# Performance work log

Measured on AMD Instinct MI355X. Metric: run time of the kernel, lower is better.

The kernel has to match this reference:

```python
import jax, jax.numpy as jnp
import numpy as np

IN_CH, OUT_CH = 384, 512


def setup_inputs() -> dict:
    key = jax.random.key(0)
    ks = jax.random.split(key, 9)
    B, C, H, W = 8, IN_CH, 48, 48
    s_in = 1.0 / np.sqrt(IN_CH)
    s_out = 1.0 / np.sqrt(OUT_CH)
    return {
        "x": jax.random.normal(ks[0], (B, C, H, W), dtype=jnp.float32),
        "Wq": jax.random.uniform(ks[1], (OUT_CH, IN_CH), jnp.float32, -s_in, s_in),
        "bq": jax.random.uniform(ks[2], (OUT_CH,), jnp.float32, -s_in, s_in),
        "Wk": jax.random.uniform(ks[3], (OUT_CH, IN_CH), jnp.float32, -s_in, s_in),
        "bk": jax.random.uniform(ks[4], (OUT_CH,), jnp.float32, -s_in, s_in),
        "Wv": jax.random.uniform(ks[5], (OUT_CH, IN_CH), jnp.float32, -s_in, s_in),
        "bv": jax.random.uniform(ks[6], (OUT_CH,), jnp.float32, -s_in, s_in),
        "Wo": jax.random.uniform(ks[7], (OUT_CH, OUT_CH), jnp.float32, -s_out, s_out),
        "bo": jax.random.uniform(ks[8], (OUT_CH,), jnp.float32, -s_out, s_out),
    }


def reference(x, Wq, bq, Wk, bk, Wv, bv, Wo, bo):
    B, C, H, W = x.shape
    N = H * W  # number of spatial tokens
    xf = x.reshape(B, C, N)  # [B, C, N]
    # 1x1 convs == per-pixel linear projections
    q = jnp.einsum('oc,bcn->bno', Wq, xf) + bq  # [B, N, O]
    k = jnp.einsum('oc,bcn->bon', Wk, xf) + bk[None, :, None]  # [B, O, N]
    v = jnp.einsum('oc,bcn->bon', Wv, xf) + bv[None, :, None]  # [B, O, N]
    scale = 1.0 / jnp.sqrt(jnp.asarray(Wq.shape[0], x.dtype))
    attn = jax.nn.softmax(jnp.einsum('bno,bom->bnm', q, k) * scale, axis=-1)  # [B, N, N]
    out = jnp.einsum('bom,bnm->bon', v, attn)  # [B, O, N]
    out = jnp.einsum('po,bon->bpn', Wo, out) + bo[None, :, None]
    return out.reshape(B, Wo.shape[0], H, W)
```

## Files before the change

kernel.cpp:

```cpp
#include <hip/hip_runtime.h>
#include <stdint.h>

#define B_    8
#define CIN   384
#define OCH   512
#define NTOK  2304
#define SCALE 0.044194173824159216f

typedef unsigned short u16;
typedef u16   u16x8 __attribute__((ext_vector_type(8)));
typedef short s16x8 __attribute__((ext_vector_type(8)));
typedef float f32x4 __attribute__((ext_vector_type(4)));

__device__ __forceinline__ u16 f2bf(float f) {
    union { uint32_t i; float f; } v; v.f = f;
    uint32_t r = v.i + 0x7fffu + ((v.i >> 16) & 1u);
    return (u16)(r >> 16);
}

typedef __attribute__((address_space(1))) const uint32_t glb_u32;
typedef __attribute__((address_space(3))) uint32_t lds_u32;

__device__ __forceinline__ void gld16(const u16* g, u16* l) {
    __builtin_amdgcn_global_load_lds((glb_u32*)g, (lds_u32*)l, 16, 0, 0);
}

__device__ __forceinline__ size_t baddr(int row, int col, int Kc) {
    return ((size_t)(row >> 4) * (Kc >> 5) + (col >> 5)) * 512
         + (size_t)(((col >> 3) & 3) * 128 + (row & 15) * 8 + (col & 7));
}

__device__ __forceinline__ void stage_blocked(const u16* __restrict__ base,
                                              int row0, int k0, int Kc,
                                              u16* __restrict__ dst, int t)
{
    const int lane = t & 63;
    const int w = t >> 6;
    const int bpr = Kc >> 5;
#pragma unroll
    for (int it = 0; it < 2; ++it) {
        const int ck = w * 2 + it;
        const u16* gp = base + ((size_t)((row0 >> 4) + ck) * bpr + (k0 >> 5)) * 512
                      + (size_t)lane * 8;
        u16* lp = dst + ck * 512;
        __builtin_amdgcn_global_load_lds((glb_u32*)gp, (lds_u32*)lp, 16, 0, 0);
    }
}

__device__ __forceinline__ void mfma_core(const u16* __restrict__ As,
                                          const u16* __restrict__ Bs,
                                          int wm16, int wn16, int lrow, int kq,
                                          f32x4 acc[4][4])
{
    s16x8 a[4], b[4];
#pragma unroll
    for (int i = 0; i < 4; ++i)
        a[i] = *(const s16x8*)(As + (((wm16 + i) * 64) + kq * 16 + lrow) * 8);
#pragma unroll
    for (int j = 0; j < 4; ++j)
        b[j] = *(const s16x8*)(Bs + (((wn16 + j) * 64) + kq * 16 + lrow) * 8);
#pragma unroll
    for (int i = 0; i < 4; ++i)
#pragma unroll
        for (int j = 0; j < 4; ++j)
            acc[i][j] = __builtin_amdgcn_mfma_f32_16x16x32_bf16(a[i], b[j], acc[i][j], 0, 0, 0);
}

template <int MODE, int K>
__device__ __forceinline__ void gemm64_core(
    u16* __restrict__ sm,
    const u16* __restrict__ A, const u16* __restrict__ Bp,
    const float* __restrict__ aux, void* __restrict__ Cout,
    int N, int m0, int n0)
{
    constexpr int NT = K / 32;
    u16* As0 = sm;
    u16* Bs0 = sm + 2048;
    u16* As1 = sm + 4096;
    u16* Bs1 = sm + 6144;

    const int ln = threadIdx.x & 63;
    const int lrow = ln & 15, kq = ln >> 4;

    const int bpr = K >> 5;
    const size_t rstep = (size_t)bpr << 9;
    const u16* pA = A  + (((size_t)(m0 >> 4) * bpr) << 9) + (size_t)(ln << 3);
    const u16* pB = Bp + (((size_t)(n0 >> 4) * bpr) << 9) + (size_t)(ln << 3);

    f32x4 acc[4][4] = {};

#define STAGE8(ga, gb, Ad, Bd)                                             \
    gld16((ga),             (Ad));        gld16((ga) + rstep,     (Ad) + 512);  \
    gld16((ga) + 2 * rstep, (Ad) + 1024); gld16((ga) + 3 * rstep, (Ad) + 1536); \
    gld16((gb),             (Bd));        gld16((gb) + rstep,     (Bd) + 512);  \
    gld16((gb) + 2 * rstep, (Bd) + 1024); gld16((gb) + 3 * rstep, (Bd) + 1536);

    STAGE8(pA, pB, As0, Bs0)

#pragma unroll 1
    for (int kt = 0; kt < NT; kt += 2) {
        STAGE8(pA + 512, pB + 512, As1, Bs1)
        asm volatile("s_waitcnt vmcnt(8)" ::: "memory");
        mfma_core(As0, Bs0, 0, 0, lrow, kq, acc);
        asm volatile("" ::: "memory");
        if (kt + 2 < NT) {
            STAGE8(pA + 1024, pB + 1024, As0, Bs0)
            asm volatile("s_waitcnt vmcnt(8)" ::: "memory");
        } else {
            asm volatile("s_waitcnt vmcnt(0)" ::: "memory");
        }
        mfma_core(As1, Bs1, 0, 0, lrow, kq, acc);
        asm volatile("" ::: "memory");
        pA += 1024; pB += 1024;
    }
#undef STAGE8

    const int offl = ((lrow >> 3) << 7) + (lrow & 7) + (kq << 5);

    if constexpr (MODE == 1) {
        u16* C = (u16*)Cout;
        float bcol[4];
#pragma unroll
        for (int j = 0; j < 4; ++j) bcol[j] = aux[n0 + j * 16 + lrow];
#pragma unroll
        for (int i = 0; i < 4; ++i) {
            u16* Crow = C + ((size_t)((m0 >> 4) + i) * (N >> 5) + (n0 >> 5)) * 512 + offl;
#pragma unroll
            for (int j = 0; j < 4; ++j) {
                u16* Cj = Crow + (j >> 1) * 512 + ((j & 1) << 8);
#pragma unroll
                for (int r = 0; r < 4; ++r)
                    Cj[r * 8] = f2bf(acc[i][j][r] + bcol[j]);
            }
        }
    } else if constexpr (MODE == 2) {
        u16* C = (u16*)Cout;
#pragma unroll
        for (int i = 0; i < 4; ++i) {
            const float4 b4 = *(const float4*)(aux + m0 + i * 16 + kq * 4);
            u16* Crow = C + ((size_t)((m0 >> 4) + i) * (N >> 5) + (n0 >> 5)) * 512 + offl;
#pragma unroll
            for (int j = 0; j < 4; ++j) {
                u16* Cj = Crow + (j >> 1) * 512 + ((j & 1) << 8);
                Cj[0]  = f2bf(acc[i][j][0] + b4.x);
                Cj[8]  = f2bf(acc[i][j][1] + b4.y);
                Cj[16] = f2bf(acc[i][j][2] + b4.z);
                Cj[24] = f2bf(acc[i][j][3] + b4.w);
            }
        }
    } else {
        float* C = (float*)Cout;
#pragma unroll
        for (int i = 0; i < 4; ++i) {
            const int row = m0 + i * 16 + kq * 4;
            const float4 b4 = *(const float4*)(aux + row);
            const float bv4[4] = {b4.x, b4.y, b4.z, b4.w};
#pragma unroll
            for (int r = 0; r < 4; ++r)
#pragma unroll
                for (int j = 0; j < 4; ++j)
                    C[(size_t)(row + r) * N + n0 + j * 16 + lrow] = acc[i][j][r] + bv4[r];
        }
    }
}

#define WQKV_SZ (OCH * CIN)
#define WO_SZ   (OCH * OCH)
#define CH_QKV  (WQKV_SZ / 8)
#define CH_WO   (WO_SZ / 8)
#define CH_TOT  (3 * CH_QKV + CH_WO)
#define PREP_BLK (CH_TOT / 256)
#define TRX_BLK  ((NTOK / 64) * (CIN / 64) * B_)

__global__ __launch_bounds__(256) void prep_kernel(
    const float* __restrict__ Wq, const float* __restrict__ Wk,
    const float* __restrict__ Wv, const float* __restrict__ Wo,
    u16* __restrict__ Wqb, u16* __restrict__ Wkb,
    u16* __restrict__ Wvb, u16* __restrict__ Wob,
    const float* __restrict__ x, u16* __restrict__ xT)
{
    __shared__ float Ts[64][66];
    const int t = threadIdx.x;

    if (blockIdx.x < PREP_BLK) {
        int lc = blockIdx.x * 256 + t;
        const float* src; u16* dst; int Kc;
        if      (lc < CH_QKV)     { src = Wq; dst = Wqb; Kc = CIN; }
        else if (lc < 2 * CH_QKV) { src = Wk; dst = Wkb; Kc = CIN; lc -= CH_QKV; }
        else if (lc < 3 * CH_QKV) { src = Wv; dst = Wvb; Kc = CIN; lc -= 2 * CH_QKV; }
        else                      { src = Wo; dst = Wob; Kc = OCH; lc -= 3 * CH_QKV; }
        const int brick = lc >> 6, l = lc & 63;
        const int bpr = Kc >> 5;
        const int g = brick / bpr, c = brick % bpr;
        const int row = g * 16 + (l & 15);
        const int col = c * 32 + (l >> 4) * 8;
        const float* s = src + (size_t)row * Kc + col;
        float4 v0 = *(const float4*)s;
        float4 v1 = *(const float4*)(s + 4);
        u16x8 o;
        o[0] = f2bf(v0.x); o[1] = f2bf(v0.y); o[2] = f2bf(v0.z); o[3] = f2bf(v0.w);
        o[4] = f2bf(v1.x); o[5] = f2bf(v1.y); o[6] = f2bf(v1.z); o[7] = f2bf(v1.w);
        *(u16x8*)(dst + (size_t)lc * 8) = o;
        return;
    }

    const int tb = blockIdx.x - PREP_BLK;
    const int n0 = (tb % 36) * 64;
    const int c0 = ((tb / 36) % 6) * 64;
    const int b  = tb / 216;
    const float* X = x + (size_t)b * CIN * NTOK;

#pragma unroll
    for (int rep = 0; rep < 4; ++rep) {
        const int cr = (t >> 4) + rep * 16;
        const int n4 = (t & 15) * 4;
        float4 v = *(const float4*)(X + (size_t)(c0 + cr) * NTOK + n0 + n4);
        *(float2*)&Ts[cr][n4]     = make_float2(v.x, v.y);
        *(float2*)&Ts[cr][n4 + 2] = make_float2(v.z, v.w);
    }
    __syncthreads();

    u16* O = xT + (size_t)b * NTOK * CIN;
#pragma unroll
    for (int rep = 0; rep < 2; ++rep) {
        const int nr = (t >> 3) + rep * 32;
        const int c8 = (t & 7) * 8;
        u16 tmp[8];
#pragma unroll
        for (int j = 0; j < 8; ++j) tmp[j] = f2bf(Ts[c8 + j][nr]);
        *(u16x8*)(O + baddr(n0 + nr, c0 + c8, CIN)) = *(const u16x8*)tmp;
    }
}

__global__ __launch_bounds__(64) void qkv64_kernel(
    const u16* __restrict__ xT,
    const u16* __restrict__ Wqb, const float* __restrict__ bq,
    const u16* __restrict__ Wkb, const float* __restrict__ bk,
    const u16* __restrict__ Wvb, const float* __restrict__ bv,
    u16* __restrict__ Qt, u16* __restrict__ Kt, u16* __restrict__ Vw)
{
    __shared__ __align__(16) u16 sm[8192];
    const int sel = blockIdx.x % 24;
    const int b = sel & 7, which = sel >> 3;
    const int rem = blockIdx.x / 24;
    const u16* xTb = xT + (size_t)b * NTOK * CIN;
    if (which < 2) {
        const int n0 = (rem & 7) * 64, m0 = (rem >> 3) * 64;
        gemm64_core<1, CIN>(sm, xTb, which ? Wkb : Wqb, which ? bk : bq,
            (which ? Kt : Qt) + (size_t)b * NTOK * OCH, OCH, m0, n0);
    } else {
        const int n0 = (rem % 36) * 64, m0 = (rem / 36) * 64;
        gemm64_core<2, CIN>(sm, Wvb, xTb, bv,
            Vw + (size_t)b * OCH * NTOK, NTOK, m0, n0);
    }
}

__global__ __launch_bounds__(256) void logits_exp_kernel(
    const u16* __restrict__ Qt, const u16* __restrict__ Kt,
    u16* __restrict__ Ew, float* __restrict__ rowsumG)
{
    const int z   = blockIdx.x % B_;
    const int rem = blockIdx.x / B_;
    const int n0 = (rem % (NTOK / 128)) * 128;
    const int m0 = (rem / (NTOK / 128)) * 128;
    const u16* A  = Qt + (size_t)z * NTOK * OCH;
    const u16* Bp = Kt + (size_t)z * NTOK * OCH;

    __shared__ u16 As[128 * 32];
    __shared__ u16 Bs[128 * 32];
    __shared__ float rowsumL[128];

    const int t = threadIdx.x;
    const int w = t >> 6, ln = t & 63;
    const int wm16 = (w & 1) * 4, wn16 = (w >> 1) * 4;
    const int lrow = ln & 15, kq = ln >> 4;

    if (t < 128) rowsumL[t] = 0.f;

    f32x4 acc[4][4] = {};

    for (int k0 = 0; k0 < OCH; k0 += 32) {
        stage_blocked(A, m0, k0, OCH, As, t);
        stage_blocked(Bp, n0, k0, OCH, Bs, t);
        __syncthreads();
        mfma_core(As, Bs, wm16, wn16, lrow, kq, acc);
        __syncthreads();
    }

    u16* E = Ew + (size_t)z * NTOK * NTOK;
    const int offl = ((lrow >> 3) << 7) + (lrow & 7) + (kq << 5);
#pragma unroll
    for (int i = 0; i < 4; ++i) {
        u16* Erow = E + ((size_t)((m0 >> 4) + wm16 + i) * (NTOK >> 5) + (n0 >> 5)) * 512 + offl;
#pragma unroll
        for (int r = 0; r < 4; ++r) {
            float part = 0.f;
#pragma unroll
            for (int j = 0; j < 4; ++j) {
                float e = __expf(acc[i][j][r] * SCALE);
                part += e;
                Erow[((wn16 + j) >> 1) * 512 + ((j & 1) << 8) + r * 8] = f2bf(e);
            }
            part += __shfl_xor(part, 1);
            part += __shfl_xor(part, 2);
            part += __shfl_xor(part, 4);
            part += __shfl_xor(part, 8);
            if (lrow == 0) atomicAdd(&rowsumL[(wm16 + i) * 16 + kq * 4 + r], part);
        }
    }
    __syncthreads();
    if (t < 128) atomicAdd(&rowsumG[(size_t)z * NTOK + m0 + t], rowsumL[t]);
}

__global__ __launch_bounds__(256) void pv_div_kernel(
    const u16* __restrict__ Ew, const u16* __restrict__ Vw,
    const float* __restrict__ rowsumG, u16* __restrict__ AOt)
{
    const int z   = blockIdx.x % B_;
    const int rem = blockIdx.x / B_;
    const int n0 = (rem % 4) * 128;
    const int m0 = (rem / 4) * 128;
    const u16* A  = Ew + (size_t)z * NTOK * NTOK;
    const u16* Bp = Vw + (size_t)z * OCH * NTOK;

    __shared__ u16 As[128 * 32];
    __shared__ u16 Bs[128 * 32];

    const int t = threadIdx.x;
    const int w = t >> 6, ln = t & 63;
    const int wm16 = (w & 1) * 4, wn16 = (w >> 1) * 4;
    const int lrow = ln & 15, kq = ln >> 4;

    f32x4 acc[4][4] = {};

    for (int k0 = 0; k0 < NTOK; k0 += 32) {
        stage_blocked(A, m0, k0, NTOK, As, t);
        stage_blocked(Bp, n0, k0, NTOK, Bs, t);
        __syncthreads();
        mfma_core(As, Bs, wm16, wn16, lrow, kq, acc);
        __syncthreads();
    }

    u16* AO = AOt + (size_t)z * NTOK * OCH;
    const int offl = ((lrow >> 3) << 7) + (lrow & 7) + (kq << 5);
#pragma unroll
    for (int i = 0; i < 4; ++i) {
        const float4 rs4 = *(const float4*)(rowsumG + (size_t)z * NTOK + m0 + (wm16 + i) * 16 + kq * 4);
        const float inv0 = 1.0f / rs4.x, inv1 = 1.0f / rs4.y;
        const float inv2 = 1.0f / rs4.z, inv3 = 1.0f / rs4.w;
        u16* Crow = AO + ((size_t)((m0 >> 4) + wm16 + i) * (OCH >> 5) + (n0 >> 5)) * 512 + offl;
#pragma unroll
        for (int j = 0; j < 4; ++j) {
            u16* Cj = Crow + ((wn16 + j) >> 1) * 512 + ((j & 1) << 8);
            Cj[0]  = f2bf(acc[i][j][0] * inv0);
            Cj[8]  = f2bf(acc[i][j][1] * inv1);
            Cj[16] = f2bf(acc[i][j][2] * inv2);
            Cj[24] = f2bf(acc[i][j][3] * inv3);
        }
    }
}

__global__ __launch_bounds__(64) void out64_kernel(
    const u16* __restrict__ Wob, const u16* __restrict__ AOt,
    const float* __restrict__ bo, float* __restrict__ out)
{
    __shared__ __align__(16) u16 sm[8192];
    const int z = blockIdx.x & 7;
    const int rem = blockIdx.x >> 3;
    const int n0 = (rem % 36) * 64, m0 = (rem / 36) * 64;
    gemm64_core<4, OCH>(sm, Wob, AOt + (size_t)z * NTOK * OCH, bo,
        out + (size_t)z * OCH * NTOK, NTOK, m0, n0);
}

extern "C" void kernel_launch(void* const* d_in, const int* in_sizes, int n_in,
                              void* d_out, int out_size, void* d_ws, size_t ws_size,
                              hipStream_t stream)
{
    const float* x  = (const float*)d_in[0];
    const float* Wq = (const float*)d_in[1];
    const float* bq = (const float*)d_in[2];
    const float* Wk = (const float*)d_in[3];
    const float* bk = (const float*)d_in[4];
    const float* Wv = (const float*)d_in[5];
    const float* bv = (const float*)d_in[6];
    const float* Wo = (const float*)d_in[7];
    const float* bo = (const float*)d_in[8];
    float* out = (float*)d_out;

    u16* ws = (u16*)d_ws;
    u16* Wqb = ws;
    u16* Wkb = Wqb + WQKV_SZ;
    u16* Wvb = Wkb + WQKV_SZ;
    u16* Wob = Wvb + WQKV_SZ;
    u16* xT  = Wob + WO_SZ;
    const size_t xtsz  = (size_t)B_ * NTOK * CIN;
    const size_t qkvsz = (size_t)B_ * NTOK * OCH;
    u16* Qt  = xT + xtsz;
    u16* Kt  = Qt + qkvsz;
    u16* Vw  = Kt + qkvsz;
    u16* Ew  = Vw + qkvsz;
    float* rowsumG = (float*)(Ew + (size_t)B_ * NTOK * NTOK);
    u16* AOt = Qt;

    dim3 blk(256), blk64(64);

    hipMemsetAsync(rowsumG, 0, (size_t)B_ * NTOK * sizeof(float), stream);

    prep_kernel<<<dim3(PREP_BLK + TRX_BLK), blk, 0, stream>>>(
        Wq, Wk, Wv, Wo, Wqb, Wkb, Wvb, Wob, x, xT);

    qkv64_kernel<<<dim3(288 * 24), blk64, 0, stream>>>(
        xT, Wqb, bq, Wkb, bk, Wvb, bv, Qt, Kt, Vw);

    logits_exp_kernel<<<dim3(18 * 18 * B_), blk, 0, stream>>>(Qt, Kt, Ew, rowsumG);

    pv_div_kernel<<<dim3(4 * 18 * B_), blk, 0, stream>>>(Ew, Vw, rowsumG, AOt);

    out64_kernel<<<dim3(288 * 8), blk64, 0, stream>>>(Wob, AOt, bo, out);
}
```

Measured before the change: 270.2 us.

## Rewrite logits kernel with 256x128 tiles, triple-buffered async LDS loads

Replaces the 128x128 logits/exp kernel with a 512-thread, 256x128-tile version. Global loads go directly to LDS through global_load_lds into three rotating buffers, prefetching two K-steps ahead and interleaving the loads with the MFMA phases under explicit waitcnt and barriers. It also raises wave priority around the MFMA bursts. The aim is to hide load latency and cut the per-step sync overhead of the old load-sync-compute loop, at the cost of about 144KB of LDS and more barriers.

```diff
diff --git a/kernel.cpp b/kernel.cpp
--- a/kernel.cpp
+++ b/kernel.cpp
@@ -255,61 +255,139 @@
     }
 }
 
-__global__ __launch_bounds__(256) void logits_exp_kernel(
+__global__ __launch_bounds__(512) void logits8p_kernel(
     const u16* __restrict__ Qt, const u16* __restrict__ Kt,
     u16* __restrict__ Ew, float* __restrict__ rowsumG)
 {
-    const int z   = blockIdx.x % B_;
-    const int rem = blockIdx.x / B_;
-    const int n0 = (rem % (NTOK / 128)) * 128;
-    const int m0 = (rem / (NTOK / 128)) * 128;
-    const u16* A  = Qt + (size_t)z * NTOK * OCH;
-    const u16* Bp = Kt + (size_t)z * NTOK * OCH;
-
-    __shared__ u16 As[128 * 32];
-    __shared__ u16 Bs[128 * 32];
-    __shared__ float rowsumL[128];
+    __shared__ __align__(16) u16 lds[3 * 24576];
+    __shared__ float rowsumL[256];
+
+    const int z = blockIdx.x & 7;
+    const int rem = blockIdx.x >> 3;
+    const int n0 = (rem % 18) * 128;
+    const int m0 = (rem / 18) * 256;
+    const u16* A = Qt + (size_t)z * NTOK * OCH;
+    const u16* B = Kt + (size_t)z * NTOK * OCH;
 
     const int t = threadIdx.x;
     const int w = t >> 6, ln = t & 63;
-    const int wm16 = (w & 1) * 4, wn16 = (w >> 1) * 4;
+    const int wr = w >> 2, wc = w & 3;
     const int lrow = ln & 15, kq = ln >> 4;
-
-    if (t < 128) rowsumL[t] = 0.f;
-
-    f32x4 acc[4][4] = {};
-
-    for (int k0 = 0; k0 < OCH; k0 += 32) {
-        stage_blocked(A, m0, k0, OCH, As, t);
-        stage_blocked(Bp, n0, k0, OCH, Bs, t);
-        __syncthreads();
-        mfma_core(As, Bs, wm16, wn16, lrow, kq, acc);
-        __syncthreads();
-    }
+    const int fo = (kq * 16 + lrow) * 8;
+
+    if (t < 256) rowsumL[t] = 0.f;
+
+    constexpr int NT = OCH / 64;
+    constexpr int bpr = OCH >> 5;
+    const int g0 = t >> 7;
+    const int cc = (t >> 6) & 1;
+    const int ll = t & 63;
+    const u16* gA = A + (((size_t)((m0 >> 4) + g0) * bpr + cc) << 9) + (size_t)(ll << 3);
+    const u16* gB = B + (((size_t)((n0 >> 4) + g0) * bpr + cc) << 9) + (size_t)(ll << 3);
+    const size_t astep = ((size_t)4 * bpr) << 9;
+    const int ldsA = (g0 << 10) + (cc << 9) + (ll << 3);
+    const int ldsB = 16384 + ldsA;
+
+#define STG_A2(buf, kt, li)                                                   \
+    { const u16* p_ = gA + (size_t)(kt) * 1024;                               \
+      gld16(p_ + (size_t)(li) * astep,       (buf) + ldsA + (li) * 4096);     \
+      gld16(p_ + (size_t)((li) + 1) * astep, (buf) + ldsA + ((li) + 1) * 4096); }
+#define STG_B2(buf, kt)                                                       \
+    { const u16* p_ = gB + (size_t)(kt) * 1024;                               \
+      gld16(p_,         (buf) + ldsB);                                        \
+      gld16(p_ + astep, (buf) + ldsB + 4096); }
+
+    STG_A2(lds, 0, 0) STG_A2(lds, 0, 2) STG_B2(lds, 0)
+    STG_A2(lds + 24576, 1, 0) STG_A2(lds + 24576, 1, 2) STG_B2(lds + 24576, 1)
+    asm volatile("s_waitcnt vmcnt(6)" ::: "memory");
+    __builtin_amdgcn_s_barrier();
+    asm volatile("" ::: "memory");
+
+    f32x4 acc[8][2] = {};
+
+    int rotC = 0;
+    int rotP = 2;
+
+#pragma unroll 1
+    for (int kt = 0; kt < NT; ++kt) {
+        u16* cur = lds + rotC * 24576;
+        u16* pre = lds + rotP * 24576;
+        const bool st = (kt + 2 < NT);
+
+        s16x8 bf[2][2];
+#pragma unroll
+        for (int j = 0; j < 2; ++j)
+#pragma unroll
+            for (int kk = 0; kk < 2; ++kk)
+                bf[j][kk] = *(const s16x8*)(cur + 16384 + (((wc * 2 + j) * 2 + kk) << 9) + fo);
+
+#pragma unroll
+        for (int p = 0; p < 4; ++p) {
+            s16x8 af[2][2];
+#pragma unroll
+            for (int i = 0; i < 2; ++i)
+#pragma unroll
+                for (int kk = 0; kk < 2; ++kk)
+                    af[i][kk] = *(const s16x8*)(cur + (((wr * 8 + p * 2 + i) * 2 + kk) << 9) + fo);
+            if (st) {
+                if (p == 0)      STG_A2(pre, kt + 2, 0)
+                else if (p == 1) STG_A2(pre, kt + 2, 2)
+                else if (p == 2) STG_B2(pre, kt + 2)
+            }
+            asm volatile("" ::: "memory");
+            __builtin_amdgcn_s_barrier();
+            asm volatile("" ::: "memory");
+            __builtin_amdgcn_s_setprio(1);
+#pragma unroll
+            for (int i = 0; i < 2; ++i)
+#pragma unroll
+                for (int j = 0; j < 2; ++j)
+#pragma unroll
+                    for (int kk = 0; kk < 2; ++kk)
+                        acc[p * 2 + i][j] = __builtin_amdgcn_mfma_f32_16x16x32_bf16(
+                            af[i][kk], bf[j][kk], acc[p * 2 + i][j], 0, 0, 0);
+            __builtin_amdgcn_s_setprio(0);
+            asm volatile("" ::: "memory");
+            __builtin_amdgcn_s_barrier();
+            asm volatile("" ::: "memory");
+        }
+        if (kt < NT - 1) {
+            if (st) asm volatile("s_waitcnt vmcnt(6)" ::: "memory");
+            else    asm volatile("s_waitcnt vmcnt(0)" ::: "memory");
+            __builtin_amdgcn_s_barrier();
+            asm volatile("" ::: "memory");
+        }
+        rotC = (rotC == 2) ? 0 : rotC + 1;
+        rotP = (rotP == 2) ? 0 : rotP + 1;
+    }
+#undef STG_A2
+#undef STG_B2
 
     u16* E = Ew + (size_t)z * NTOK * NTOK;
-    const int offl = ((lrow >> 3) << 7) + (lrow & 7) + (kq << 5);
-#pragma unroll
-    for (int i = 0; i < 4; ++i) {
-        u16* Erow = E + ((size_t)((m0 >> 4) + wm16 + i) * (NTOK >> 5) + (n0 >> 5)) * 512 + offl;
+    float* rsG = rowsumG + (size_t)z * NTOK;
+#pragma unroll
+    for (int i8 = 0; i8 < 8; ++i8) {
+        u16* Erow = E + ((size_t)((m0 >> 4) + wr * 8 + i8) * (NTOK >> 5) + (n0 >> 5) + wc) * 512
+                  + (lrow & 7);
 #pragma unroll
         for (int r = 0; r < 4; ++r) {
             float part = 0.f;
 #pragma unroll
-            for (int j = 0; j < 4; ++j) {
-                float e = __expf(acc[i][j][r] * SCALE);
+            for (int j = 0; j < 2; ++j) {
+                float e = __expf(acc[i8][j][r] * SCALE);
                 part += e;
-                Erow[((wn16 + j) >> 1) * 512 + ((j & 1) << 8) + r * 8] = f2bf(e);
+                Erow[(j * 2 + (lrow >> 3)) * 128 + (kq * 4 + r) * 8] = f2bf(e);
             }
             part += __shfl_xor(part, 1);
             part += __shfl_xor(part, 2);
             part += __shfl_xor(part, 4);
             part += __shfl_xor(part, 8);
-            if (lrow == 0) atomicAdd(&rowsumL[(wm16 + i) * 16 + kq * 4 + r], part);
+            if (lrow == 0)
+                atomicAdd(&rowsumL[(wr * 8 + i8) * 16 + kq * 4 + r], part);
         }
     }
     __syncthreads();
-    if (t < 128) atomicAdd(&rowsumG[(size_t)z * NTOK + m0 + t], rowsumL[t]);
+    if (t < 256) atomicAdd(&rsG[m0 + t], rowsumL[t]);
 }
 
 __global__ __launch_bounds__(256) void pv_div_kernel(
@@ -402,9 +480,9 @@
     float* rowsumG = (float*)(Ew + (size_t)B_ * NTOK * NTOK);
     u16* AOt = Qt;
 
-    dim3 blk(256), blk64(64);
-
-    hipMemsetAsync(rowsumG, 0, (size_t)B_ * NTOK * sizeof(float), stream);
+    dim3 blk(256), blk64(64), blk512(512);
+
+    (void)hipMemsetAsync(rowsumG, 0, (size_t)B_ * NTOK * sizeof(float), stream);
 
     prep_kernel<<<dim3(PREP_BLK + TRX_BLK), blk, 0, stream>>>(
         Wq, Wk, Wv, Wo, Wqb, Wkb, Wvb, Wob, x, xT);
@@ -412,7 +490,7 @@
     qkv64_kernel<<<dim3(288 * 24), blk64, 0, stream>>>(
         xT, Wqb, bq, Wkb, bk, Wvb, bv, Qt, Kt, Vw);
 
-    logits_exp_kernel<<<dim3(18 * 18 * B_), blk, 0, stream>>>(Qt, Kt, Ew, rowsumG);
+    logits8p_kernel<<<dim3(162 * 8), blk512, 0, stream>>>(Qt, Kt, Ew, rowsumG);
 
     pv_div_kernel<<<dim3(4 * 18 * B_), blk, 0, stream>>>(Ew, Vw, rowsumG, AOt);
 
```

Result: slower. 305.7 us (+13.1%).
